# Optimization experiments

Hardware: AMD Instinct MI355X
Metric: run time of the kernel (lower is better)

## Reference

```python
import jax, jax.numpy as jnp
import numpy as np

B, T, F, H, L = 128, 256, 1024, 1024, 2

def setup_inputs() -> dict:
    key = jax.random.key(0)
    ks = jax.random.split(key, 9)
    s_in = 1.0 / np.sqrt(F)
    s_h = 1.0 / np.sqrt(H)
    return {
        "x": jax.random.normal(ks[0], (B, T, F), jnp.float32),
        "W_ih0": jax.random.normal(ks[1], (4 * H, F), jnp.float32) * s_in,
        "b_ih0": jax.random.normal(ks[2], (4 * H,), jnp.float32) * s_in,
        "W_hh0": jax.random.normal(ks[3], (4 * H, H), jnp.float32) * s_h,
        "b_hh0": jax.random.normal(ks[4], (4 * H,), jnp.float32) * s_h,
        "W_ih1": jax.random.normal(ks[5], (4 * H, H), jnp.float32) * s_h,
        "b_ih1": jax.random.normal(ks[6], (4 * H,), jnp.float32) * s_h,
        "W_hh1": jax.random.normal(ks[7], (4 * H, H), jnp.float32) * s_h,
        "b_hh1": jax.random.normal(ks[8], (4 * H,), jnp.float32) * s_h,
    }

def _cell(x_t, h, c, W_ih, b_ih, W_hh, b_hh):
    # gates: (B, 4H); chunk order i, f, g, o (matches torch .chunk(4, dim=1))
    gates = x_t @ W_ih.T + b_ih + h @ W_hh.T + b_hh
    i, f, g, o = jnp.split(gates, 4, axis=1)
    i = jax.nn.sigmoid(i)
    f = jax.nn.sigmoid(f)
    g = jnp.tanh(g)
    o = jax.nn.sigmoid(o)
    c_new = f * c + i * g
    h_new = o * jnp.tanh(c_new)
    return h_new, c_new

def reference(x, W_ih0, b_ih0, W_hh0, b_hh0, W_ih1, b_ih1, W_hh1, b_hh1):
    Bv = x.shape[0]
    z = jnp.zeros((Bv, H), x.dtype)
    init = (z, z, z, z)  # h0, c0, h1, c1

    def step(carry, x_t):
        h0, c0, h1, c1 = carry
        h0, c0 = _cell(x_t, h0, c0, W_ih0, b_ih0, W_hh0, b_hh0)
        h1, c1 = _cell(h0, h1, c1, W_ih1, b_ih1, W_hh1, b_hh1)
        return (h0, c0, h1, c1), h1

    # scan over time: xs shaped (T, B, F)
    _, ys = jax.lax.scan(step, init, jnp.swapaxes(x, 0, 1))
    return jnp.swapaxes(ys, 0, 1)  # (B, T, H)
```

## Files before the change

### kernel.cpp

```cpp
#include <hip/hip_runtime.h>

#define B_ 128
#define T_ 256
#define F_ 1024
#define H_ 1024

typedef __bf16 bf16x8 __attribute__((ext_vector_type(8)));
typedef __bf16 bf16x4 __attribute__((ext_vector_type(4)));
typedef float f32x4 __attribute__((ext_vector_type(4)));

#define WROW 2056

__device__ __forceinline__ float sigf(float v)  { return 1.0f / (1.0f + __expf(-v)); }
__device__ __forceinline__ float tanhfast(float x) { return 1.0f - 2.0f / (1.0f + __expf(2.0f * x)); }

__global__ void k_cvt(const float* __restrict__ src, __bf16* __restrict__ dst, int n) {
    int i = (blockIdx.x * 256 + threadIdx.x) * 8;
    if (i + 7 < n) {
        float4 a = *(const float4*)(src + i);
        float4 b = *(const float4*)(src + i + 4);
        bf16x8 o = { (__bf16)a.x, (__bf16)a.y, (__bf16)a.z, (__bf16)a.w,
                     (__bf16)b.x, (__bf16)b.y, (__bf16)b.z, (__bf16)b.w };
        *(bf16x8*)(dst + i) = o;
    }
}

__global__ void k_init(__bf16* h0b, __bf16* h1b, unsigned* bar) {
    int i = blockIdx.x * 256 + threadIdx.x;
    h0b[i] = (__bf16)0.0f;
    h1b[i] = (__bf16)0.0f;
    if (i < 64) bar[i] = 0u;
}

#define STEP(A0, A1, KW) do { \
    bf16x8 b0_ = *(const bf16x8*)&wB[lrow][(KW) + quad * 8]; \
    bf16x8 b1_ = *(const bf16x8*)&wB[16 + lrow][(KW) + quad * 8]; \
    acc00 = __builtin_amdgcn_mfma_f32_16x16x32_bf16(A0, b0_, acc00, 0, 0, 0); \
    acc01 = __builtin_amdgcn_mfma_f32_16x16x32_bf16(A0, b1_, acc01, 0, 0, 0); \
    acc10 = __builtin_amdgcn_mfma_f32_16x16x32_bf16(A1, b0_, acc10, 0, 0, 0); \
    acc11 = __builtin_amdgcn_mfma_f32_16x16x32_bf16(A1, b1_, acc11, 0, 0, 0); \
} while (0)

#define KLOOP_BF16(SRC, STRIDE, WBASE) do { \
    const __bf16* pa_ = (SRC) + (long)arow0 * (STRIDE) + kbase + quad * 8; \
    const __bf16* pb_ = (SRC) + (long)arow1 * (STRIDE) + kbase + quad * 8; \
    bf16x8 ra_[8], rb_[8]; \
    _Pragma("unroll") \
    for (int i_ = 0; i_ < 8; ++i_) { \
        ra_[i_] = *(const bf16x8*)(pa_ + i_ * 32); \
        rb_[i_] = *(const bf16x8*)(pb_ + i_ * 32); \
    } \
    _Pragma("unroll") \
    for (int ks_ = 0; ks_ < 16; ++ks_) { \
        bf16x8 a0_ = ra_[ks_ & 7]; \
        bf16x8 a1_ = rb_[ks_ & 7]; \
        if (ks_ < 8) { \
            ra_[ks_ & 7] = *(const bf16x8*)(pa_ + (ks_ + 8) * 32); \
            rb_[ks_ & 7] = *(const bf16x8*)(pb_ + (ks_ + 8) * 32); \
        } \
        STEP(a0_, a1_, (WBASE) + kbase + ks_ * 32); \
    } \
} while (0)

#define KLOOP_F32(SRC, STRIDE, WBASE) do { \
    const float* pa_ = (SRC) + (long)arow0 * (STRIDE) + kbase + quad * 8; \
    const float* pb_ = (SRC) + (long)arow1 * (STRIDE) + kbase + quad * 8; \
    float4 rA_[4], rB_[4], rC_[4], rD_[4]; \
    _Pragma("unroll") \
    for (int i_ = 0; i_ < 4; ++i_) { \
        rA_[i_] = *(const float4*)(pa_ + i_ * 32); \
        rB_[i_] = *(const float4*)(pa_ + i_ * 32 + 4); \
        rC_[i_] = *(const float4*)(pb_ + i_ * 32); \
        rD_[i_] = *(const float4*)(pb_ + i_ * 32 + 4); \
    } \
    _Pragma("unroll") \
    for (int ks_ = 0; ks_ < 16; ++ks_) { \
        float4 va_ = rA_[ks_ & 3], vb_ = rB_[ks_ & 3]; \
        float4 vc_ = rC_[ks_ & 3], vd_ = rD_[ks_ & 3]; \
        if (ks_ < 12) { \
            rA_[ks_ & 3] = *(const float4*)(pa_ + (ks_ + 4) * 32); \
            rB_[ks_ & 3] = *(const float4*)(pa_ + (ks_ + 4) * 32 + 4); \
            rC_[ks_ & 3] = *(const float4*)(pb_ + (ks_ + 4) * 32); \
            rD_[ks_ & 3] = *(const float4*)(pb_ + (ks_ + 4) * 32 + 4); \
        } \
        bf16x8 a0_ = { (__bf16)va_.x, (__bf16)va_.y, (__bf16)va_.z, (__bf16)va_.w, \
                       (__bf16)vb_.x, (__bf16)vb_.y, (__bf16)vb_.z, (__bf16)vb_.w }; \
        bf16x8 a1_ = { (__bf16)vc_.x, (__bf16)vc_.y, (__bf16)vc_.z, (__bf16)vc_.w, \
                       (__bf16)vd_.x, (__bf16)vd_.y, (__bf16)vd_.z, (__bf16)vd_.w }; \
        STEP(a0_, a1_, (WBASE) + kbase + ks_ * 32); \
    } \
} while (0)

#define ZACC() do { \
    acc00 = (f32x4){0.f,0.f,0.f,0.f}; acc01 = (f32x4){0.f,0.f,0.f,0.f}; \
    acc10 = (f32x4){0.f,0.f,0.f,0.f}; acc11 = (f32x4){0.f,0.f,0.f,0.f}; \
} while (0)

#define EPI(MT, ACC_A, ACC_B, HW, TT, WOUT) \
    _Pragma("unroll") \
    for (int r = 0; r < 4; ++r) { \
        float v0 = (ACC_A)[r], v1 = (ACC_B)[r]; \
        float q0 = __shfl_xor(v0, 8); \
        float q1 = __shfl_xor(v1, 8); \
        float iv = (hi ? q0 : v0) + bi; \
        float fv = (hi ? v0 : q0) + bf_; \
        float gv = (hi ? q1 : v1) + bg; \
        float ov = (hi ? v1 : q1) + bo; \
        float cn = sigf(fv) * creg[MT][r] + sigf(iv) * tanhfast(gv); \
        creg[MT][r] = cn; \
        float hn = sigf(ov) * tanhfast(cn); \
        if (!hi) { \
            const int b = (wave << 5) + (MT) * 16 + (quad << 2) + r; \
            (HW)[(long)b * H_ + j0 + jj] = (__bf16)hn; \
            if (WOUT) out[((long)b * T_ + (TT)) * H_ + j0 + jj] = hn; \
        } \
    }

#define REDUCE_EPI(HW, TT, WOUT) do { \
    if (wave >= 4) { \
        _Pragma("unroll") \
        for (int i_ = 0; i_ < 4; ++i_) { \
            red[wave - 4][i_     ][lane] = acc00[i_]; \
            red[wave - 4][i_ + 4 ][lane] = acc01[i_]; \
            red[wave - 4][i_ + 8 ][lane] = acc10[i_]; \
            red[wave - 4][i_ + 12][lane] = acc11[i_]; \
        } \
    } \
    __syncthreads(); \
    if (wave < 4) { \
        _Pragma("unroll") \
        for (int i_ = 0; i_ < 4; ++i_) { \
            acc00[i_] += red[wave][i_     ][lane]; \
            acc01[i_] += red[wave][i_ + 4 ][lane]; \
            acc10[i_] += red[wave][i_ + 8 ][lane]; \
            acc11[i_] += red[wave][i_ + 12][lane]; \
        } \
        const float bi  = bb[jj]; \
        const float bf_ = bb[8 + jj]; \
        const float bg  = bb[16 + jj]; \
        const float bo  = bb[24 + jj]; \
        EPI(0, acc00, acc01, HW, TT, WOUT); \
        EPI(1, acc10, acc11, HW, TT, WOUT); \
    } \
} while (0)

__global__ __launch_bounds__(512, 1) void lstm_persist(
    const float* __restrict__ x,
    const float* __restrict__ Wih0, const float* __restrict__ Whh0,
    const float* __restrict__ Wih1, const float* __restrict__ Whh1,
    const float* __restrict__ bih0, const float* __restrict__ bhh0,
    const float* __restrict__ bih1, const float* __restrict__ bhh1,
    __bf16* __restrict__ h0a, __bf16* __restrict__ h0b,
    __bf16* __restrict__ h1a, __bf16* __restrict__ h1b,
    unsigned* bar, const __bf16* __restrict__ xb, float* __restrict__ out)
{
    const int cell = blockIdx.x >> 7;
    const int cidx = blockIdx.x & 127;
    const int j0   = cidx << 3;

    __shared__ __align__(16) __bf16 wB[32][WROW];
    __shared__ __align__(16) float  red[4][16][64];
    __shared__ float bb[32];

    const int tid  = threadIdx.x;
    const int wave = tid >> 6;
    const int lane = tid & 63;
    const int quad = lane >> 4;
    const int lrow = lane & 15;
    const int jj   = lane & 7;
    const bool hi  = (lane & 8) != 0;

    const int kbase = (wave >> 2) << 9;
    const int arow0 = ((wave & 3) << 5) + lrow;
    const int arow1 = arow0 + 16;

    unsigned* cnt = bar;
    unsigned* gen = bar + 32;

    const float* Wih = cell ? Wih1 : Wih0;
    const float* Whh = cell ? Whh1 : Whh0;

    for (int e = tid; e < 32 * 512; e += 512) {
        int n  = e >> 9;
        int k  = (e & 511) << 2;
        int wr = ((n >> 3) << 10) + j0 + (n & 7);
        const float* src = (k < 1024) ? (Wih + (long)wr * 1024 + k)
                                      : (Whh + (long)wr * 1024 + (k - 1024));
        float4 v = *(const float4*)src;
        bf16x4 o = { (__bf16)v.x, (__bf16)v.y, (__bf16)v.z, (__bf16)v.w };
        *(bf16x4*)&wB[n][k] = o;
    }
    if (tid < 32) {
        int wr = ((tid >> 3) << 10) + j0 + (tid & 7);
        bb[tid] = cell ? (bih1[wr] + bhh1[wr]) : (bih0[wr] + bhh0[wr]);
    }
    __syncthreads();

    float creg[2][4] = {};
    f32x4 acc00, acc01, acc10, acc11;
    ZACC();

    if (cell == 0) {
        if (xb) KLOOP_BF16(xb + 0, (long)T_ * F_, 0);
        else    KLOOP_F32 (x  + 0, (long)T_ * F_, 0);
    }

    for (int p = 0; p <= T_; ++p) {
        if (cell == 0) {
            if (p < T_) {
                const int t = p;
                const __bf16* hprev = (t & 1) ? h0a : h0b;
                __bf16* hw          = (t & 1) ? h0b : h0a;
                KLOOP_BF16(hprev, H_, 1024);
                REDUCE_EPI(hw, t, false);
            }
        } else {
            if (p >= 1) {
                const int t = p - 1;
                ZACC();
                const __bf16* s0 = (t & 1) ? h0b : h0a;
                const __bf16* s1 = (t & 1) ? h1a : h1b;
                __bf16* hw       = (t & 1) ? h1b : h1a;
                KLOOP_BF16(s0, H_, 0);
                KLOOP_BF16(s1, H_, 1024);
                REDUCE_EPI(hw, t, true);
            }
        }

        if (p < T_) {
            __syncthreads();
            unsigned g = 0;
            if (tid == 0) {
                __threadfence();
                g = __hip_atomic_load(gen, __ATOMIC_RELAXED, __HIP_MEMORY_SCOPE_AGENT);
                unsigned a = __hip_atomic_fetch_add(cnt, 1u, __ATOMIC_RELAXED,
                                                    __HIP_MEMORY_SCOPE_AGENT);
                if (a == 255u) {
                    __hip_atomic_store(cnt, 0u, __ATOMIC_RELAXED, __HIP_MEMORY_SCOPE_AGENT);
                    __hip_atomic_store(gen, g + 1u, __ATOMIC_RELEASE, __HIP_MEMORY_SCOPE_AGENT);
                }
            }
            if (cell == 0) {
                ZACC();
                if (p + 1 < T_) {
                    if (xb) KLOOP_BF16(xb + (long)(p + 1) * F_, (long)T_ * F_, 0);
                    else    KLOOP_F32 (x  + (long)(p + 1) * F_, (long)T_ * F_, 0);
                }
            }
            if (tid == 0) {
                for (;;) {
                    bool done = false;
                    for (int it = 0; it < 256; ++it) {
                        if (__hip_atomic_load(gen, __ATOMIC_RELAXED,
                                              __HIP_MEMORY_SCOPE_AGENT) != g) { done = true; break; }
                        __builtin_amdgcn_s_sleep(2);
                    }
                    if (done) break;
                    if (__hip_atomic_load(gen, __ATOMIC_ACQUIRE,
                                          __HIP_MEMORY_SCOPE_AGENT) != g) break;
                }
                __builtin_amdgcn_fence(__ATOMIC_ACQUIRE, "agent");
            }
            __syncthreads();
        }
    }
}

extern "C" void kernel_launch(void* const* d_in, const int* in_sizes, int n_in,
                              void* d_out, int out_size, void* d_ws, size_t ws_size,
                              hipStream_t stream)
{
    const float* x    = (const float*)d_in[0];
    const float* Wih0 = (const float*)d_in[1];
    const float* bih0 = (const float*)d_in[2];
    const float* Whh0 = (const float*)d_in[3];
    const float* bhh0 = (const float*)d_in[4];
    const float* Wih1 = (const float*)d_in[5];
    const float* bih1 = (const float*)d_in[6];
    const float* Whh1 = (const float*)d_in[7];
    const float* bhh1 = (const float*)d_in[8];
    float* out = (float*)d_out;

    char* ws = (char*)d_ws;
    unsigned* bar = (unsigned*)ws;
    __bf16* h0a = (__bf16*)(ws + 4096);
    __bf16* h0b = (__bf16*)(ws + 4096 + (256 << 10));
    __bf16* h1a = (__bf16*)(ws + 4096 + (512 << 10));
    __bf16* h1b = (__bf16*)(ws + 4096 + (768 << 10));
    const __bf16* xb = nullptr;

    const size_t XB_OFF = 4096 + (1 << 20);
    if (ws_size >= XB_OFF + ((size_t)64 << 20)) {
        __bf16* xbw = (__bf16*)(ws + XB_OFF);
        k_cvt<<<dim3(16384), dim3(256), 0, stream>>>(x, xbw, B_ * T_ * F_);
        xb = xbw;
    }
    k_init<<<dim3(512), dim3(256), 0, stream>>>(h0b, h1b, bar);

    void* args[] = {
        (void*)&x, (void*)&Wih0, (void*)&Whh0, (void*)&Wih1, (void*)&Whh1,
        (void*)&bih0, (void*)&bhh0, (void*)&bih1, (void*)&bhh1,
        (void*)&h0a, (void*)&h0b, (void*)&h1a, (void*)&h1b,
        (void*)&bar, (void*)&xb, (void*)&out
    };
    hipError_t err = hipLaunchCooperativeKernel((const void*)lstm_persist,
                                                dim3(256), dim3(512), args, 0, stream);
    if (err != hipSuccess) {
        lstm_persist<<<dim3(256), dim3(512), 0, stream>>>(
            x, Wih0, Whh0, Wih1, Whh1, bih0, bhh0, bih1, bhh1,
            h0a, h0b, h1a, h1b, bar, xb, out);
    }
    (void)in_sizes; (void)n_in; (void)out_size;
}
```

Baseline: 7.376 ms.

## Precompute layer-0 input projection as a batched GEMM and use a hierarchical barrier

Adds a k_xproj kernel that computes x@W_ih0 for all timesteps up front with MFMA and stores it in a blocked layout. The persistent recurrent kernel then adds this precomputed slice in its epilogue instead of running the per-step x projection loop. Hidden-state buffers move to a blocked layout so per-step K-loop loads are contiguous, and the grid barrier becomes a two-level counter tree with monotonic generations. The cost is a large workspace requirement (256-512 MB) and an extra memory-heavy kernel before the recurrence.

```diff
diff --git a/kernel.cpp b/kernel.cpp
--- a/kernel.cpp
+++ b/kernel.cpp
@@ -10,6 +10,7 @@
 typedef float f32x4 __attribute__((ext_vector_type(4)));
 
 #define WROW 2056
+#define XLDA 72
 
 __device__ __forceinline__ float sigf(float v)  { return 1.0f / (1.0f + __expf(-v)); }
 __device__ __forceinline__ float tanhfast(float x) { return 1.0f - 2.0f / (1.0f + __expf(2.0f * x)); }
@@ -29,7 +30,72 @@
     int i = blockIdx.x * 256 + threadIdx.x;
     h0b[i] = (__bf16)0.0f;
     h1b[i] = (__bf16)0.0f;
-    if (i < 64) bar[i] = 0u;
+    if (i < 256) bar[i] = 0u;
+}
+
+__global__ __launch_bounds__(256) void k_xproj(
+    const __bf16* __restrict__ xb, const float* __restrict__ Wih0,
+    float* __restrict__ xpf, __bf16* __restrict__ xpb)
+{
+    const int t   = blockIdx.x >> 7;
+    const int sub = blockIdx.x & 127;
+    const int m0  = (sub & 1) * 64;
+    const int n0  = (sub >> 1) * 64;
+
+    __shared__ __align__(16) __bf16 lsA[64 * XLDA];
+    __shared__ __align__(16) __bf16 lsB[64 * XLDA];
+
+    const int tid  = threadIdx.x;
+    const int wave = tid >> 6;
+    const int lane = tid & 63;
+    const int quad = lane >> 4;
+    const int lrow = lane & 15;
+
+    f32x4 a0 = {0,0,0,0}, a1 = {0,0,0,0}, a2 = {0,0,0,0}, a3 = {0,0,0,0};
+
+    for (int kt = 0; kt < 1024; kt += 64) {
+        #pragma unroll
+        for (int i = 0; i < 2; ++i) {
+            int idx = tid + i * 256;
+            int r = idx >> 3, s = idx & 7;
+            *(uint4*)&lsA[r * XLDA + s * 8] =
+                *(const uint4*)(xb + ((long)(m0 + r) * T_ + t) * F_ + kt + s * 8);
+        }
+        #pragma unroll
+        for (int i = 0; i < 4; ++i) {
+            int idx = tid + i * 256;
+            int r = idx >> 4, s = idx & 15;
+            float4 v = *(const float4*)(Wih0 + (long)(n0 + r) * F_ + kt + s * 4);
+            bf16x4 o = { (__bf16)v.x, (__bf16)v.y, (__bf16)v.z, (__bf16)v.w };
+            *(bf16x4*)&lsB[r * XLDA + s * 4] = o;
+        }
+        __syncthreads();
+        #pragma unroll
+        for (int ki = 0; ki < 64; ki += 32) {
+            bf16x8 af = *(const bf16x8*)&lsA[(wave * 16 + lrow) * XLDA + ki + quad * 8];
+            bf16x8 b0 = *(const bf16x8*)&lsB[( 0 + lrow) * XLDA + ki + quad * 8];
+            bf16x8 b1 = *(const bf16x8*)&lsB[(16 + lrow) * XLDA + ki + quad * 8];
+            bf16x8 b2 = *(const bf16x8*)&lsB[(32 + lrow) * XLDA + ki + quad * 8];
+            bf16x8 b3 = *(const bf16x8*)&lsB[(48 + lrow) * XLDA + ki + quad * 8];
+            a0 = __builtin_amdgcn_mfma_f32_16x16x32_bf16(af, b0, a0, 0, 0, 0);
+            a1 = __builtin_amdgcn_mfma_f32_16x16x32_bf16(af, b1, a1, 0, 0, 0);
+            a2 = __builtin_amdgcn_mfma_f32_16x16x32_bf16(af, b2, a2, 0, 0, 0);
+            a3 = __builtin_amdgcn_mfma_f32_16x16x32_bf16(af, b3, a3, 0, 0, 0);
+        }
+        __syncthreads();
+    }
+
+    const long xbase = (long)t * 524288;
+    #define XSTORE(NT, ACC) { \
+        int n = n0 + (NT) * 16 + lrow; int g = n >> 10; int jc = n & 1023; \
+        long off = xbase + (long)(jc >> 3) * 4096 + (long)b * 32 + g * 8 + (jc & 7); \
+        if (xpf) xpf[off] = (ACC)[r]; else xpb[off] = (__bf16)(ACC)[r]; }
+    #pragma unroll
+    for (int r = 0; r < 4; ++r) {
+        const int b = m0 + wave * 16 + quad * 4 + r;
+        XSTORE(0, a0) XSTORE(1, a1) XSTORE(2, a2) XSTORE(3, a3)
+    }
+    #undef XSTORE
 }
 
 #define STEP(A0, A1, KW) do { \
@@ -41,48 +107,36 @@
     acc11 = __builtin_amdgcn_mfma_f32_16x16x32_bf16(A1, b1_, acc11, 0, 0, 0); \
 } while (0)
 
-#define KLOOP_BF16(SRC, STRIDE, WBASE) do { \
-    const __bf16* pa_ = (SRC) + (long)arow0 * (STRIDE) + kbase + quad * 8; \
-    const __bf16* pb_ = (SRC) + (long)arow1 * (STRIDE) + kbase + quad * 8; \
-    bf16x8 ra_[8], rb_[8]; \
-    _Pragma("unroll") \
-    for (int i_ = 0; i_ < 8; ++i_) { \
-        ra_[i_] = *(const bf16x8*)(pa_ + i_ * 32); \
-        rb_[i_] = *(const bf16x8*)(pb_ + i_ * 32); \
-    } \
+#define KLOOP_H(SRC, WBASE) do { \
+    const __bf16* ph_ = (SRC) + ((long)((kbase >> 3) + quad)) * 1024 + arow0 * 8; \
     _Pragma("unroll") \
     for (int ks_ = 0; ks_ < 16; ++ks_) { \
-        bf16x8 a0_ = ra_[ks_ & 7]; \
-        bf16x8 a1_ = rb_[ks_ & 7]; \
-        if (ks_ < 8) { \
-            ra_[ks_ & 7] = *(const bf16x8*)(pa_ + (ks_ + 8) * 32); \
-            rb_[ks_ & 7] = *(const bf16x8*)(pb_ + (ks_ + 8) * 32); \
-        } \
+        bf16x8 a0_ = *(const bf16x8*)(ph_ + ks_ * 4096); \
+        bf16x8 a1_ = *(const bf16x8*)(ph_ + ks_ * 4096 + 128); \
         STEP(a0_, a1_, (WBASE) + kbase + ks_ * 32); \
     } \
 } while (0)
 
-#define KLOOP_F32(SRC, STRIDE, WBASE) do { \
-    const float* pa_ = (SRC) + (long)arow0 * (STRIDE) + kbase + quad * 8; \
-    const float* pb_ = (SRC) + (long)arow1 * (STRIDE) + kbase + quad * 8; \
-    float4 rA_[4], rB_[4], rC_[4], rD_[4]; \
-    _Pragma("unroll") \
-    for (int i_ = 0; i_ < 4; ++i_) { \
-        rA_[i_] = *(const float4*)(pa_ + i_ * 32); \
-        rB_[i_] = *(const float4*)(pa_ + i_ * 32 + 4); \
-        rC_[i_] = *(const float4*)(pb_ + i_ * 32); \
-        rD_[i_] = *(const float4*)(pb_ + i_ * 32 + 4); \
-    } \
+#define KLOOP_RM(SRC, S, WBASE) do { \
+    const __bf16* pa_ = (SRC) + (long)arow0 * (S) + kbase + quad * 8; \
+    const __bf16* pb_ = (SRC) + (long)arow1 * (S) + kbase + quad * 8; \
     _Pragma("unroll") \
     for (int ks_ = 0; ks_ < 16; ++ks_) { \
-        float4 va_ = rA_[ks_ & 3], vb_ = rB_[ks_ & 3]; \
-        float4 vc_ = rC_[ks_ & 3], vd_ = rD_[ks_ & 3]; \
-        if (ks_ < 12) { \
-            rA_[ks_ & 3] = *(const float4*)(pa_ + (ks_ + 4) * 32); \
-            rB_[ks_ & 3] = *(const float4*)(pa_ + (ks_ + 4) * 32 + 4); \
-            rC_[ks_ & 3] = *(const float4*)(pb_ + (ks_ + 4) * 32); \
-            rD_[ks_ & 3] = *(const float4*)(pb_ + (ks_ + 4) * 32 + 4); \
-        } \
+        bf16x8 a0_ = *(const bf16x8*)(pa_ + ks_ * 32); \
+        bf16x8 a1_ = *(const bf16x8*)(pb_ + ks_ * 32); \
+        STEP(a0_, a1_, (WBASE) + kbase + ks_ * 32); \
+    } \
+} while (0)
+
+#define KLOOP_F32(SRC, S, WBASE) do { \
+    const float* pa_ = (SRC) + (long)arow0 * (S) + kbase + quad * 8; \
+    const float* pb_ = (SRC) + (long)arow1 * (S) + kbase + quad * 8; \
+    _Pragma("unroll") \
+    for (int ks_ = 0; ks_ < 16; ++ks_) { \
+        float4 va_ = *(const float4*)(pa_ + ks_ * 32); \
+        float4 vb_ = *(const float4*)(pa_ + ks_ * 32 + 4); \
+        float4 vc_ = *(const float4*)(pb_ + ks_ * 32); \
+        float4 vd_ = *(const float4*)(pb_ + ks_ * 32 + 4); \
         bf16x8 a0_ = { (__bf16)va_.x, (__bf16)va_.y, (__bf16)va_.z, (__bf16)va_.w, \
                        (__bf16)vb_.x, (__bf16)vb_.y, (__bf16)vb_.z, (__bf16)vb_.w }; \
         bf16x8 a1_ = { (__bf16)vc_.x, (__bf16)vc_.y, (__bf16)vc_.z, (__bf16)vc_.w, \
@@ -94,6 +148,17 @@
 #define ZACC() do { \
     acc00 = (f32x4){0.f,0.f,0.f,0.f}; acc01 = (f32x4){0.f,0.f,0.f,0.f}; \
     acc10 = (f32x4){0.f,0.f,0.f,0.f}; acc11 = (f32x4){0.f,0.f,0.f,0.f}; \
+} while (0)
+
+#define XPADD(P) do { \
+    _Pragma("unroll") \
+    for (int r_ = 0; r_ < 4; ++r_) { \
+        int b0_ = (wave << 5) + (quad << 2) + r_; \
+        acc00[r_] += (float)(P)[b0_ * 32 + lrow]; \
+        acc01[r_] += (float)(P)[b0_ * 32 + 16 + lrow]; \
+        acc10[r_] += (float)(P)[(b0_ + 16) * 32 + lrow]; \
+        acc11[r_] += (float)(P)[(b0_ + 16) * 32 + 16 + lrow]; \
+    } \
 } while (0)
 
 #define EPI(MT, ACC_A, ACC_B, HW, TT, WOUT) \
@@ -111,12 +176,12 @@
         float hn = sigf(ov) * tanhfast(cn); \
         if (!hi) { \
             const int b = (wave << 5) + (MT) * 16 + (quad << 2) + r; \
-            (HW)[(long)b * H_ + j0 + jj] = (__bf16)hn; \
+            (HW)[b * 8 + jj] = (__bf16)hn; \
             if (WOUT) out[((long)b * T_ + (TT)) * H_ + j0 + jj] = hn; \
         } \
     }
 
-#define REDUCE_EPI(HW, TT, WOUT) do { \
+#define REDUCE_EPI(HW, TT, WOUT, XOFF) do { \
     if (wave >= 4) { \
         _Pragma("unroll") \
         for (int i_ = 0; i_ < 4; ++i_) { \
@@ -135,6 +200,10 @@
             acc10[i_] += red[wave][i_ + 8 ][lane]; \
             acc11[i_] += red[wave][i_ + 12][lane]; \
         } \
+        if ((XOFF) >= 0) { \
+            if (xpf)      { const float*  xp_ = xpf + (XOFF); XPADD(xp_); } \
+            else          { const __bf16* xp_ = xpb + (XOFF); XPADD(xp_); } \
+        } \
         const float bi  = bb[jj]; \
         const float bf_ = bb[8 + jj]; \
         const float bg  = bb[16 + jj]; \
@@ -152,7 +221,9 @@
     const float* __restrict__ bih1, const float* __restrict__ bhh1,
     __bf16* __restrict__ h0a, __bf16* __restrict__ h0b,
     __bf16* __restrict__ h1a, __bf16* __restrict__ h1b,
-    unsigned* bar, const __bf16* __restrict__ xb, float* __restrict__ out)
+    unsigned* bar, const __bf16* __restrict__ xb,
+    const float* __restrict__ xpf, const __bf16* __restrict__ xpb,
+    float* __restrict__ out)
 {
     const int cell = blockIdx.x >> 7;
     const int cidx = blockIdx.x & 127;
@@ -173,9 +244,7 @@
     const int kbase = (wave >> 2) << 9;
     const int arow0 = ((wave & 3) << 5) + lrow;
     const int arow1 = arow0 + 16;
-
-    unsigned* cnt = bar;
-    unsigned* gen = bar + 32;
+    const bool hasxp = (xpf != nullptr) || (xpb != nullptr);
 
     const float* Wih = cell ? Wih1 : Wih0;
     const float* Whh = cell ? Whh1 : Whh0;
@@ -200,9 +269,9 @@
     f32x4 acc00, acc01, acc10, acc11;
     ZACC();
 
-    if (cell == 0) {
-        if (xb) KLOOP_BF16(xb + 0, (long)T_ * F_, 0);
-        else    KLOOP_F32 (x  + 0, (long)T_ * F_, 0);
+    if (cell == 0 && !hasxp) {
+        if (xb) KLOOP_RM(xb + 0, (long)T_ * F_, 0);
+        else    KLOOP_F32(x + 0, (long)T_ * F_, 0);
     }
 
     for (int p = 0; p <= T_; ++p) {
@@ -210,9 +279,11 @@
             if (p < T_) {
                 const int t = p;
                 const __bf16* hprev = (t & 1) ? h0a : h0b;
-                __bf16* hw          = (t & 1) ? h0b : h0a;
-                KLOOP_BF16(hprev, H_, 1024);
-                REDUCE_EPI(hw, t, false);
+                __bf16* hw = ((t & 1) ? h0b : h0a) + cidx * 1024;
+                if (hasxp) ZACC();
+                KLOOP_H(hprev, 1024);
+                const long xoff = hasxp ? (((long)t * 128 + cidx) * 4096) : -1;
+                REDUCE_EPI(hw, t, false, xoff);
             }
         } else {
             if (p >= 1) {
@@ -220,44 +291,46 @@
                 ZACC();
                 const __bf16* s0 = (t & 1) ? h0b : h0a;
                 const __bf16* s1 = (t & 1) ? h1a : h1b;
-                __bf16* hw       = (t & 1) ? h1b : h1a;
-                KLOOP_BF16(s0, H_, 0);
-                KLOOP_BF16(s1, H_, 1024);
-                REDUCE_EPI(hw, t, true);
+                __bf16* hw = ((t & 1) ? h1b : h1a) + cidx * 1024;
+                KLOOP_H(s0, 0);
+                KLOOP_H(s1, 1024);
+                REDUCE_EPI(hw, t, true, (long)-1);
             }
         }
 
         if (p < T_) {
             __syncthreads();
-            unsigned g = 0;
+            const unsigned genv = (unsigned)(p + 1);
             if (tid == 0) {
                 __threadfence();
-                g = __hip_atomic_load(gen, __ATOMIC_RELAXED, __HIP_MEMORY_SCOPE_AGENT);
-                unsigned a = __hip_atomic_fetch_add(cnt, 1u, __ATOMIC_RELAXED,
-                                                    __HIP_MEMORY_SCOPE_AGENT);
-                if (a == 255u) {
-                    __hip_atomic_store(cnt, 0u, __ATOMIC_RELAXED, __HIP_MEMORY_SCOPE_AGENT);
-                    __hip_atomic_store(gen, g + 1u, __ATOMIC_RELEASE, __HIP_MEMORY_SCOPE_AGENT);
+                unsigned v = __hip_atomic_fetch_add(&bar[(blockIdx.x & 7) << 4], 1u,
+                                 __ATOMIC_RELAXED, __HIP_MEMORY_SCOPE_AGENT) + 1u;
+                if (v == 32u * genv) {
+                    unsigned r = __hip_atomic_fetch_add(&bar[128], 1u,
+                                     __ATOMIC_RELAXED, __HIP_MEMORY_SCOPE_AGENT) + 1u;
+                    if (r == 8u * genv)
+                        __hip_atomic_store(&bar[136], genv,
+                                           __ATOMIC_RELEASE, __HIP_MEMORY_SCOPE_AGENT);
                 }
             }
-            if (cell == 0) {
+            if (cell == 0 && !hasxp) {
                 ZACC();
                 if (p + 1 < T_) {
-                    if (xb) KLOOP_BF16(xb + (long)(p + 1) * F_, (long)T_ * F_, 0);
-                    else    KLOOP_F32 (x  + (long)(p + 1) * F_, (long)T_ * F_, 0);
+                    if (xb) KLOOP_RM(xb + (long)(p + 1) * F_, (long)T_ * F_, 0);
+                    else    KLOOP_F32(x + (long)(p + 1) * F_, (long)T_ * F_, 0);
                 }
             }
             if (tid == 0) {
                 for (;;) {
                     bool done = false;
-                    for (int it = 0; it < 256; ++it) {
-                        if (__hip_atomic_load(gen, __ATOMIC_RELAXED,
-                                              __HIP_MEMORY_SCOPE_AGENT) != g) { done = true; break; }
-                        __builtin_amdgcn_s_sleep(2);
+                    for (int it = 0; it < 128; ++it) {
+                        if (__hip_atomic_load(&bar[136], __ATOMIC_RELAXED,
+                                __HIP_MEMORY_SCOPE_AGENT) >= genv) { done = true; break; }
+                        __builtin_amdgcn_s_sleep(1);
                     }
                     if (done) break;
-                    if (__hip_atomic_load(gen, __ATOMIC_ACQUIRE,
-                                          __HIP_MEMORY_SCOPE_AGENT) != g) break;
+                    if (__hip_atomic_load(&bar[136], __ATOMIC_ACQUIRE,
+                            __HIP_MEMORY_SCOPE_AGENT) >= genv) break;
                 }
                 __builtin_amdgcn_fence(__ATOMIC_ACQUIRE, "agent");
             }
@@ -287,28 +360,37 @@
     __bf16* h0b = (__bf16*)(ws + 4096 + (256 << 10));
     __bf16* h1a = (__bf16*)(ws + 4096 + (512 << 10));
     __bf16* h1b = (__bf16*)(ws + 4096 + (768 << 10));
-    const __bf16* xb = nullptr;
 
     const size_t XB_OFF = 4096 + (1 << 20);
-    if (ws_size >= XB_OFF + ((size_t)64 << 20)) {
+    const size_t XP_OFF = XB_OFF + ((size_t)64 << 20);
+    const __bf16* xb  = nullptr;
+    float*  xpf = nullptr;
+    __bf16* xpb = nullptr;
+
+    if (ws_size >= XP_OFF) {
         __bf16* xbw = (__bf16*)(ws + XB_OFF);
         k_cvt<<<dim3(16384), dim3(256), 0, stream>>>(x, xbw, B_ * T_ * F_);
         xb = xbw;
+        if (ws_size >= XP_OFF + ((size_t)512 << 20))       xpf = (float*)(ws + XP_OFF);
+        else if (ws_size >= XP_OFF + ((size_t)256 << 20))  xpb = (__bf16*)(ws + XP_OFF);
+        if (xpf || xpb)
+            k_xproj<<<dim3(32768), dim3(256), 0, stream>>>(xb, Wih0, xpf, xpb);
     }
     k_init<<<dim3(512), dim3(256), 0, stream>>>(h0b, h1b, bar);
 
+    const float* xpf_c = xpf; const __bf16* xpb_c = xpb;
     void* args[] = {
         (void*)&x, (void*)&Wih0, (void*)&Whh0, (void*)&Wih1, (void*)&Whh1,
         (void*)&bih0, (void*)&bhh0, (void*)&bih1, (void*)&bhh1,
         (void*)&h0a, (void*)&h0b, (void*)&h1a, (void*)&h1b,
-        (void*)&bar, (void*)&xb, (void*)&out
+        (void*)&bar, (void*)&xb, (void*)&xpf_c, (void*)&xpb_c, (void*)&out
     };
     hipError_t err = hipLaunchCooperativeKernel((const void*)lstm_persist,
                                                 dim3(256), dim3(512), args, 0, stream);
     if (err != hipSuccess) {
         lstm_persist<<<dim3(256), dim3(512), 0, stream>>>(
             x, Wih0, Whh0, Wih1, Whh1, bih0, bhh0, bih1, bhh1,
-            h0a, h0b, h1a, h1b, bar, xb, out);
+            h0a, h0b, h1a, h1b, bar, xb, xpf_c, xpb_c, out);
     }
     (void)in_sizes; (void)n_in; (void)out_size;
 }
```

Result: faster. 6.672 ms (-9.5%).
